# Kernel optimization log

Measured on AMD Instinct MI355X. Metric: run time of the kernel, lower is better.

Reference implementation:

```python
import jax, jax.numpy as jnp
import numpy as np

N = 131072        # minibatch nodes
T = 100000        # rows per featured type table
D = 512           # raw feature dim for featured types
E = 256           # embedding size
NUM_NODES = 262144  # total nodes in graph (node embedding table rows)


def setup_inputs() -> dict:
    key = jax.random.key(0)
    ks = jax.random.split(key, 8)
    return {
        "node_ids": jax.random.randint(ks[0], (N,), 0, NUM_NODES),
        "node_tids": jax.random.randint(ks[1], (N,), 0, 4),
        "type_ids": jax.random.randint(ks[2], (N,), 0, T),
        "feats0": jax.random.normal(ks[3], (T, D), dtype=jnp.float32),
        "feats1": jax.random.normal(ks[4], (T, D), dtype=jnp.float32),
        "W0": jax.random.normal(ks[5], (D, E), dtype=jnp.float32) * (6.0 / (D + E)) ** 0.5,
        "W1": jax.random.normal(ks[6], (D, E), dtype=jnp.float32) * (6.0 / (D + E)) ** 0.5,
        "node_emb": jax.random.uniform(ks[7], (NUM_NODES, E), dtype=jnp.float32, minval=-1.0, maxval=1.0),
    }


def reference(node_ids, node_tids, type_ids, feats0, feats1, W0, W1, node_emb):
    # Per-type dispatch: types 0,1 have raw features projected by W_t;
    # types 2,3 read the learnable node-embedding table.
    m0 = (node_tids == 0)
    m1 = (node_tids == 1)
    # safe gather indices (masked-out rows read row 0, then zeroed)
    y0 = (feats0[jnp.where(m0, type_ids, 0)] @ W0) * m0[:, None].astype(W0.dtype)
    y1 = (feats1[jnp.where(m1, type_ids, 0)] @ W1) * m1[:, None].astype(W1.dtype)
    m_emb = jnp.logical_not(m0 | m1)
    ye = node_emb[node_ids] * m_emb[:, None].astype(node_emb.dtype)
    return y0 + y1 + ye  # [N, E]
```

## Files before the change

### kernel.cpp

```cpp
#include <hip/hip_runtime.h>
#include <hip/hip_bf16.h>

typedef __attribute__((ext_vector_type(4))) float f32x4;
typedef __attribute__((ext_vector_type(8))) short bf16x8;

#define NN 131072
#define TT 100000
#define DD 512
#define EE 256
#define NT_MAX 1026

__device__ inline ushort f2bf(float f) {
    union { float f; unsigned u; } x; x.f = f;
    unsigned r = x.u + 0x7fffu + ((x.u >> 16) & 1u);
    return (ushort)(r >> 16);
}

__device__ inline void gload16(const void* g, void* l) {
    __builtin_amdgcn_global_load_lds(
        (const __attribute__((address_space(1))) unsigned int*)g,
        (__attribute__((address_space(3))) unsigned int*)l, 16, 0, 0);
}

__global__ void prep_w_kernel(const float* __restrict__ W0, const float* __restrict__ W1,
                              ushort* __restrict__ Wt0, ushort* __restrict__ Wt1,
                              int* __restrict__ cnt) {
    if (blockIdx.x == 0 && threadIdx.x < 4) cnt[threadIdx.x] = 0;
    int gid = blockIdx.x * 256 + threadIdx.x;
    int t = gid >> 15;
    int rem = gid & 32767;
    int d = rem >> 6, eg = rem & 63;
    const float* W = t ? W1 : W0;
    ushort* Wt = t ? Wt1 : Wt0;
    f32x4 v = *(const f32x4*)(W + d * EE + eg * 4);
#pragma unroll
    for (int j = 0; j < 4; ++j)
        Wt[(size_t)(eg * 4 + j) * DD + d] = f2bf(v[j]);
}

__global__ void compact_kernel(const int* __restrict__ tids, int* __restrict__ cnt,
                               int* __restrict__ l0, int* __restrict__ l1) {
    const int i = blockIdx.x * 256 + threadIdx.x;
    const int t = tids[i];
    const int lane = threadIdx.x & 63, wid = threadIdx.x >> 6;
    unsigned long long b0 = __ballot(t == 0);
    unsigned long long b1 = __ballot(t == 1);
    __shared__ int w0[4], w1[4];
    __shared__ int base0, base1;
    if (lane == 0) { w0[wid] = __popcll(b0); w1[wid] = __popcll(b1); }
    __syncthreads();
    if (threadIdx.x == 0) {
        base0 = atomicAdd(&cnt[0], w0[0] + w0[1] + w0[2] + w0[3]);
        base1 = atomicAdd(&cnt[1], w1[0] + w1[1] + w1[2] + w1[3]);
    }
    __syncthreads();
    int p0 = 0, p1 = 0;
#pragma unroll
    for (int w = 0; w < 4; ++w) if (w < wid) { p0 += w0[w]; p1 += w1[w]; }
    const unsigned long long ltm = (1ull << lane) - 1ull;
    if (t == 0)      l0[base0 + p0 + __popcll(b0 & ltm)] = i;
    else if (t == 1) l1[base1 + p1 + __popcll(b1 & ltm)] = i;
}

__global__ void emb_gather_kernel(const int* __restrict__ ids, const int* __restrict__ tids,
                                  const float* __restrict__ emb, float* __restrict__ out) {
    int gid = blockIdx.x * 256 + threadIdx.x;
    int i = gid >> 6, j = gid & 63;
    if (tids[i] >= 2) {
        ((f32x4*)out)[(size_t)i * 64 + j] = ((const f32x4*)emb)[(size_t)ids[i] * 64 + j];
    }
}

__global__ __launch_bounds__(512, 4) void gemm_gather_kernel(
    const int* __restrict__ l0, const int* __restrict__ l1,
    const int* __restrict__ cntp, const int* __restrict__ type_ids,
    const float* __restrict__ feats0, const float* __restrict__ feats1,
    const ushort* __restrict__ Wt0, const ushort* __restrict__ Wt1,
    float* __restrict__ out) {
    const int cnt0 = cntp[0], cnt1 = cntp[1];
    const int nt0 = (cnt0 + 127) >> 7;
    const int nt1 = (cnt1 + 127) >> 7;
    const int b = blockIdx.x;
    const int* list; const float* feats; const ushort* Wt; int cnt, tile;
    if (b < nt0)             { tile = b;       list = l0; feats = feats0; Wt = Wt0; cnt = cnt0; }
    else if (b < nt0 + nt1)  { tile = b - nt0; list = l1; feats = feats1; Wt = Wt1; cnt = cnt1; }
    else return;
    const int row0 = tile * 128;

    __shared__ char Alds[2][32768];
    __shared__ char Blds[2][32768];

    const int tid = threadIdx.x;
    const int lane = tid & 63, wid = tid >> 6;
    const int wr = wid >> 1, wc = wid & 1;
    const int ln15 = lane & 15, lq = lane >> 4;

    const float* asrc[4];
#pragma unroll
    for (int p = 0; p < 4; ++p) {
        int rp = p * 32 + (tid >> 4);
        int rg = row0 + rp;
        int g = (rg < cnt) ? type_ids[list[rg]] : 0;
        int lchunk = ((tid >> 1) & 7) ^ (rp & 7);
        asrc[p] = feats + (size_t)g * DD + lchunk * 8 + (tid & 1) * 4;
    }
    const ushort* bsrc[4];
#pragma unroll
    for (int p = 0; p < 4; ++p) {
        int d = p * 8192 + tid * 16;
        int col = d >> 7;
        int seg = ((d >> 4) & 7) ^ (col & 7);
        bsrc[p] = Wt + (size_t)col * DD + seg * 8;
    }

    auto stage = [&](int buf, int k0) {
#pragma unroll
        for (int p = 0; p < 4; ++p)
            gload16(asrc[p] + k0, &Alds[buf][p * 8192 + wid * 1024]);
#pragma unroll
        for (int p = 0; p < 4; ++p)
            gload16(bsrc[p] + k0, &Blds[buf][p * 8192 + wid * 1024]);
    };

    f32x4 acc[2][8] = {};

    stage(0, 0);
    __syncthreads();

    for (int kk = 0; kk < 8; ++kk) {
        const int cur = kk & 1;
        if (kk < 7) stage(cur ^ 1, (kk + 1) * 64);

#pragma unroll
        for (int kh = 0; kh < 2; ++kh) {
            const int kb = kh * 64 + lq * 16;
            const int ch = kh * 4 + lq;
            const int ra0 = wr * 32 + ln15;
            const int ra1 = ra0 + 16;
            const char* a0p = &Alds[cur][ra0 * 256 + ((ch ^ (ra0 & 7)) << 5)];
            const char* a1p = &Alds[cur][ra1 * 256 + ((ch ^ (ra1 & 7)) << 5)];
            f32x4 a0lo = *(const f32x4*)a0p, a0hi = *(const f32x4*)(a0p + 16);
            f32x4 a1lo = *(const f32x4*)a1p, a1hi = *(const f32x4*)(a1p + 16);
            bf16x8 A0, A1;
#pragma unroll
            for (int j = 0; j < 4; ++j) {
                A0[j]     = (short)f2bf(a0lo[j]);
                A0[j + 4] = (short)f2bf(a0hi[j]);
                A1[j]     = (short)f2bf(a1lo[j]);
                A1[j + 4] = (short)f2bf(a1hi[j]);
            }
#pragma unroll
            for (int ni = 0; ni < 8; ++ni) {
                int col = wc * 128 + ni * 16 + ln15;
                int baddr = (col * 128 + kb) ^ ((col & 7) << 4);
                bf16x8 bfr = *(const bf16x8*)(&Blds[cur][baddr]);
                acc[0][ni] = __builtin_amdgcn_mfma_f32_16x16x32_bf16(A0, bfr, acc[0][ni], 0, 0, 0);
                acc[1][ni] = __builtin_amdgcn_mfma_f32_16x16x32_bf16(A1, bfr, acc[1][ni], 0, 0, 0);
            }
        }
        __syncthreads();
    }

#pragma unroll
    for (int mi = 0; mi < 2; ++mi) {
        int mbase = row0 + wr * 32 + mi * 16 + lq * 4;
#pragma unroll
        for (int rr = 0; rr < 4; ++rr) {
            int r = mbase + rr;
            if (r < cnt) {
                int nd = list[r];
                float* orow = out + (size_t)nd * EE + wc * 128 + ln15;
#pragma unroll
                for (int ni = 0; ni < 8; ++ni) orow[ni * 16] = acc[mi][ni][rr];
            }
        }
    }
}

extern "C" void kernel_launch(void* const* d_in, const int* in_sizes, int n_in,
                              void* d_out, int out_size, void* d_ws, size_t ws_size,
                              hipStream_t stream) {
    const int*   node_ids  = (const int*)d_in[0];
    const int*   node_tids = (const int*)d_in[1];
    const int*   type_ids  = (const int*)d_in[2];
    const float* feats0    = (const float*)d_in[3];
    const float* feats1    = (const float*)d_in[4];
    const float* W0        = (const float*)d_in[5];
    const float* W1        = (const float*)d_in[6];
    const float* node_emb  = (const float*)d_in[7];
    float* out = (float*)d_out;

    char* ws = (char*)d_ws;
    int* cnt = (int*)ws;
    int* l0  = (int*)(ws + 16);
    int* l1  = (int*)(ws + 16 + 524288);
    ushort* Wt0 = (ushort*)(ws + 16 + 2 * 524288);
    ushort* Wt1 = Wt0 + DD * EE;

    prep_w_kernel<<<256, 256, 0, stream>>>(W0, W1, Wt0, Wt1, cnt);
    compact_kernel<<<512, 256, 0, stream>>>(node_tids, cnt, l0, l1);
    emb_gather_kernel<<<32768, 256, 0, stream>>>(node_ids, node_tids, node_emb, out);
    gemm_gather_kernel<<<NT_MAX, 512, 0, stream>>>(l0, l1, cnt, type_ids,
                                                   feats0, feats1, Wt0, Wt1, out);
}
```

Measured before the change: 133.3 us.

## Deepen GEMM pipeline to four-stage K=32 buffers with vmcnt-based waits

Replaces the double-buffered K=64 staging in the gather GEMM with a four-deep ring of K=32 buffers, keeping three loads in flight and synchronizing through explicit s_waitcnt vmcnt plus barrier instead of __syncthreads. The LDS swizzle layouts for A and B are redone for the narrower tiles, and the occupancy hint in launch_bounds is dropped. The goal is to hide gather latency from the random feature-row loads. The cost is more barriers per K step and less MFMA work between them.

```diff
diff --git a/kernel.cpp b/kernel.cpp
--- a/kernel.cpp
+++ b/kernel.cpp
@@ -21,6 +21,12 @@
         (const __attribute__((address_space(1))) unsigned int*)g,
         (__attribute__((address_space(3))) unsigned int*)l, 16, 0, 0);
 }
+
+#define WAIT_BAR(N) do {                                   \
+    asm volatile("s_waitcnt vmcnt(" #N ")" ::: "memory");  \
+    __builtin_amdgcn_s_barrier();                          \
+    __builtin_amdgcn_sched_barrier(0);                     \
+} while (0)
 
 __global__ void prep_w_kernel(const float* __restrict__ W0, const float* __restrict__ W1,
                               ushort* __restrict__ Wt0, ushort* __restrict__ Wt1,
@@ -71,7 +77,7 @@
     }
 }
 
-__global__ __launch_bounds__(512, 4) void gemm_gather_kernel(
+__global__ __launch_bounds__(512) void gemm_gather_kernel(
     const int* __restrict__ l0, const int* __restrict__ l1,
     const int* __restrict__ cntp, const int* __restrict__ type_ids,
     const float* __restrict__ feats0, const float* __restrict__ feats1,
@@ -87,79 +93,77 @@
     else return;
     const int row0 = tile * 128;
 
-    __shared__ char Alds[2][32768];
-    __shared__ char Blds[2][32768];
+    __shared__ char Alds[4][16384];
+    __shared__ char Blds[4][16384];
 
     const int tid = threadIdx.x;
     const int lane = tid & 63, wid = tid >> 6;
     const int wr = wid >> 1, wc = wid & 1;
     const int ln15 = lane & 15, lq = lane >> 4;
 
-    const float* asrc[4];
-#pragma unroll
-    for (int p = 0; p < 4; ++p) {
-        int rp = p * 32 + (tid >> 4);
-        int rg = row0 + rp;
+    const float* asrc[2];
+#pragma unroll
+    for (int p = 0; p < 2; ++p) {
+        int row = p * 64 + (tid >> 3);
+        int rg = row0 + row;
         int g = (rg < cnt) ? type_ids[list[rg]] : 0;
-        int lchunk = ((tid >> 1) & 7) ^ (rp & 7);
-        asrc[p] = feats + (size_t)g * DD + lchunk * 8 + (tid & 1) * 4;
-    }
-    const ushort* bsrc[4];
-#pragma unroll
-    for (int p = 0; p < 4; ++p) {
-        int d = p * 8192 + tid * 16;
-        int col = d >> 7;
-        int seg = ((d >> 4) & 7) ^ (col & 7);
-        bsrc[p] = Wt + (size_t)col * DD + seg * 8;
-    }
-
-    auto stage = [&](int buf, int k0) {
-#pragma unroll
-        for (int p = 0; p < 4; ++p)
-            gload16(asrc[p] + k0, &Alds[buf][p * 8192 + wid * 1024]);
-#pragma unroll
-        for (int p = 0; p < 4; ++p)
-            gload16(bsrc[p] + k0, &Blds[buf][p * 8192 + wid * 1024]);
+        int hl = (tid & 7) ^ (row & 7);
+        asrc[p] = feats + (size_t)g * DD + hl * 4;
+    }
+    const ushort* bsrc[2];
+#pragma unroll
+    for (int p = 0; p < 2; ++p) {
+        int col = p * 128 + (tid >> 2);
+        int sl = (tid & 3) ^ ((col ^ (col >> 2)) & 3);
+        bsrc[p] = Wt + (size_t)col * DD + sl * 8;
+    }
+
+    auto stage = [&](int buf, int kk) {
+        gload16(asrc[0] + kk * 32, &Alds[buf][tid * 16]);
+        gload16(asrc[1] + kk * 32, &Alds[buf][8192 + tid * 16]);
+        gload16(bsrc[0] + kk * 32, &Blds[buf][tid * 16]);
+        gload16(bsrc[1] + kk * 32, &Blds[buf][8192 + tid * 16]);
     };
 
     f32x4 acc[2][8] = {};
 
-    stage(0, 0);
-    __syncthreads();
-
-    for (int kk = 0; kk < 8; ++kk) {
-        const int cur = kk & 1;
-        if (kk < 7) stage(cur ^ 1, (kk + 1) * 64);
-
-#pragma unroll
-        for (int kh = 0; kh < 2; ++kh) {
-            const int kb = kh * 64 + lq * 16;
-            const int ch = kh * 4 + lq;
-            const int ra0 = wr * 32 + ln15;
-            const int ra1 = ra0 + 16;
-            const char* a0p = &Alds[cur][ra0 * 256 + ((ch ^ (ra0 & 7)) << 5)];
-            const char* a1p = &Alds[cur][ra1 * 256 + ((ch ^ (ra1 & 7)) << 5)];
-            f32x4 a0lo = *(const f32x4*)a0p, a0hi = *(const f32x4*)(a0p + 16);
-            f32x4 a1lo = *(const f32x4*)a1p, a1hi = *(const f32x4*)(a1p + 16);
-            bf16x8 A0, A1;
-#pragma unroll
-            for (int j = 0; j < 4; ++j) {
-                A0[j]     = (short)f2bf(a0lo[j]);
-                A0[j + 4] = (short)f2bf(a0hi[j]);
-                A1[j]     = (short)f2bf(a1lo[j]);
-                A1[j + 4] = (short)f2bf(a1hi[j]);
-            }
-#pragma unroll
-            for (int ni = 0; ni < 8; ++ni) {
-                int col = wc * 128 + ni * 16 + ln15;
-                int baddr = (col * 128 + kb) ^ ((col & 7) << 4);
-                bf16x8 bfr = *(const bf16x8*)(&Blds[cur][baddr]);
-                acc[0][ni] = __builtin_amdgcn_mfma_f32_16x16x32_bf16(A0, bfr, acc[0][ni], 0, 0, 0);
-                acc[1][ni] = __builtin_amdgcn_mfma_f32_16x16x32_bf16(A1, bfr, acc[1][ni], 0, 0, 0);
-            }
+    auto compute = [&](int buf) {
+        const char* Ab = Alds[buf];
+        const char* Bb = Blds[buf];
+        const int ra0 = wr * 32 + ln15, ra1 = ra0 + 16;
+        const int h0 = lq * 2, h1 = h0 + 1;
+        f32x4 a0lo = *(const f32x4*)(Ab + ra0 * 128 + ((h0 ^ (ra0 & 7)) << 4));
+        f32x4 a0hi = *(const f32x4*)(Ab + ra0 * 128 + ((h1 ^ (ra0 & 7)) << 4));
+        f32x4 a1lo = *(const f32x4*)(Ab + ra1 * 128 + ((h0 ^ (ra1 & 7)) << 4));
+        f32x4 a1hi = *(const f32x4*)(Ab + ra1 * 128 + ((h1 ^ (ra1 & 7)) << 4));
+        bf16x8 A0, A1;
+#pragma unroll
+        for (int j = 0; j < 4; ++j) {
+            A0[j]     = (short)f2bf(a0lo[j]);
+            A0[j + 4] = (short)f2bf(a0hi[j]);
+            A1[j]     = (short)f2bf(a1lo[j]);
+            A1[j + 4] = (short)f2bf(a1hi[j]);
         }
-        __syncthreads();
-    }
+#pragma unroll
+        for (int ni = 0; ni < 8; ++ni) {
+            int col = wc * 128 + ni * 16 + ln15;
+            int baddr = col * 64 + ((lq ^ ((col ^ (col >> 2)) & 3)) << 4);
+            bf16x8 bfr = *(const bf16x8*)(Bb + baddr);
+            acc[0][ni] = __builtin_amdgcn_mfma_f32_16x16x32_bf16(A0, bfr, acc[0][ni], 0, 0, 0);
+            acc[1][ni] = __builtin_amdgcn_mfma_f32_16x16x32_bf16(A1, bfr, acc[1][ni], 0, 0, 0);
+        }
+    };
+
+    stage(0, 0); stage(1, 1); stage(2, 2);
+
+    for (int kk = 0; kk < 13; ++kk) {
+        WAIT_BAR(8);
+        stage((kk + 3) & 3, kk + 3);
+        compute(kk & 3);
+    }
+    WAIT_BAR(8);  compute(1);
+    WAIT_BAR(4);  compute(2);
+    WAIT_BAR(0);  compute(3);
 
 #pragma unroll
     for (int mi = 0; mi < 2; ++mi) {
```

Result: slower. 149.9 us (+12.4%).
